# Optimization experiments

Measured on AMD Instinct MI355X. Metric: run time of the kernel, lower is better.

Reference implementation:

```python
import jax, jax.numpy as jnp
import numpy as np

DIM = 256
NEG_SLOPE = 0.01  # torch F.leaky_relu default


def setup_inputs() -> dict:
    key = jax.random.key(0)
    ks = jax.random.split(key, 10)
    B, O, I, D = 16, 64, 512, DIM
    q = jax.random.normal(ks[0], (B, O, D), dtype=jnp.float32)
    k = jax.random.normal(ks[1], (B, I, D), dtype=jnp.float32)
    v = jax.random.normal(ks[2], (B, I, D), dtype=jnp.float32)
    mask = jax.random.randint(ks[3], (B, I), 0, 2).astype(bool)  # 1/True = pad
    s = 1.0 / np.sqrt(2 * D)
    # score MLP: Linear(2D -> D), tanh, Linear(D -> 1)
    W1 = jax.random.normal(ks[4], (D, 2 * D), dtype=jnp.float32) * s
    b1 = jnp.zeros((D,), dtype=jnp.float32)
    W2 = jax.random.normal(ks[5], (1, D), dtype=jnp.float32) * (1.0 / np.sqrt(D))
    b2 = jnp.zeros((1,), dtype=jnp.float32)
    # output projection fw: Linear(D -> D)
    Wf = jax.random.normal(ks[6], (D, D), dtype=jnp.float32) * (1.0 / np.sqrt(D))
    bf = jnp.zeros((D,), dtype=jnp.float32)
    return {"q": q, "k": k, "v": v, "mask": mask,
            "W1": W1, "b1": b1, "W2": W2, "b2": b2, "Wf": Wf, "bf": bf}


def reference(q, k, v, mask, W1, b1, W2, b2, Wf, bf):
    # Linear over concat([q, k]) decomposes exactly: W1 @ [q;k] = W1q@q + W1k@k
    D = q.shape[-1]
    W1q, W1k = W1[:, :D], W1[:, D:]
    qp = jnp.einsum('bod,hd->boh', q, W1q)          # (B, O, D)
    kp = jnp.einsum('bid,hd->bih', k, W1k)          # (B, I, D)
    h = jnp.tanh(qp[:, :, None, :] + kp[:, None, :, :] + b1)  # (B, O, I, D)
    score = jnp.einsum('boih,h->boi', h, W2[0]) + b2[0]       # (B, O, I)
    score = jnp.where(mask[:, None, :], -jnp.inf, score)
    attn = jax.nn.softmax(score, axis=-1)           # (B, O, I)
    out = jnp.einsum('boi,bid->bod', attn, v)       # (B, O, D)
    out = out @ Wf.T + bf                           # dropout in eval mode = identity
    out = jnp.where(out >= 0, out, NEG_SLOPE * out) # leaky_relu
    return out, attn
```

## Files before the change

kernel.cpp:

```cpp
#include <hip/hip_runtime.h>
#include <math.h>

#define DIM 256
#define BATCH 16
#define NO 64
#define NI 512
#define NEG_SLOPE 0.01f
#define CSCALE 2.885390081777927f
#define OT 2

__global__ __launch_bounds__(256, 4) void proj_kernel(
    const float* __restrict__ q, const float* __restrict__ k,
    const float* __restrict__ W1, const float* __restrict__ b1,
    const float* __restrict__ Wf,
    float* __restrict__ Eq, float* __restrict__ Ek4, float* __restrict__ WfT)
{
  __shared__ float smem[8704];

  const int t  = threadIdx.x;
  const int bx = blockIdx.x;

  if (bx >= 576) {
    const int tt = bx - 576;
    const int tr = tt >> 2, tc = tt & 3;
#pragma unroll
    for (int p = 0; p < 4; ++p) {
      int idx = p * 256 + t;
      int row = idx >> 4, j = idx & 15;
      float4 vv = *(const float4*)(Wf + (size_t)(tr * 64 + row) * 256 + tc * 64 + j * 4);
      *(float4*)&smem[row * 68 + j * 4] = vv;
    }
    __syncthreads();
#pragma unroll
    for (int p = 0; p < 4; ++p) {
      int idx = p * 256 + t;
      int row = idx >> 4, j = idx & 15;
      float4 ov;
      ov.x = smem[(j * 4 + 0) * 68 + row];
      ov.y = smem[(j * 4 + 1) * 68 + row];
      ov.z = smem[(j * 4 + 2) * 68 + row];
      ov.w = smem[(j * 4 + 3) * 68 + row];
      *(float4*)(WfT + (size_t)(tc * 64 + row) * 256 + tr * 64 + j * 4) = ov;
    }
    return;
  }

  float* At = smem;
  float* Wt = smem + 4352;

  const int tx = t & 15;
  const int ty = t >> 4;
  const int mt = bx >> 2;
  const int nt = bx & 3;
  const int r0 = mt * 64;
  const int h0 = nt * 64;
  const bool isq = (r0 < BATCH * NO);
  const float* src = isq ? (q + (size_t)r0 * DIM)
                         : (k + (size_t)(r0 - BATCH * NO) * DIM);
  const int coff = isq ? 0 : DIM;

  float acc[4][4] = {};

  for (int c0 = 0; c0 < DIM; c0 += 64) {
    __syncthreads();
#pragma unroll
    for (int p = 0; p < 4; ++p) {
      int idx = p * 256 + t;
      int row = idx >> 4, j = idx & 15;
      float4 av = *(const float4*)(src + (size_t)row * DIM + c0 + j * 4);
      At[(4 * j + 0) * 68 + row] = av.x;
      At[(4 * j + 1) * 68 + row] = av.y;
      At[(4 * j + 2) * 68 + row] = av.z;
      At[(4 * j + 3) * 68 + row] = av.w;
      float4 wv = *(const float4*)(W1 + (size_t)(h0 + row) * (2 * DIM) + coff + c0 + j * 4);
      Wt[(4 * j + 0) * 68 + row] = wv.x;
      Wt[(4 * j + 1) * 68 + row] = wv.y;
      Wt[(4 * j + 2) * 68 + row] = wv.z;
      Wt[(4 * j + 3) * 68 + row] = wv.w;
    }
    __syncthreads();
#pragma unroll
    for (int dk = 0; dk < 64; ++dk) {
      float4 a4 = *(const float4*)&At[dk * 68 + ty * 4];
      float4 w4 = *(const float4*)&Wt[dk * 68 + tx * 4];
      const float ar[4] = {a4.x, a4.y, a4.z, a4.w};
      const float wr[4] = {w4.x, w4.y, w4.z, w4.w};
#pragma unroll
      for (int rr = 0; rr < 4; ++rr)
#pragma unroll
        for (int cc = 0; cc < 4; ++cc)
          acc[rr][cc] = fmaf(ar[rr], wr[cc], acc[rr][cc]);
    }
  }

  if (isq) {
    float4 bv = *(const float4*)(b1 + h0 + tx * 4);
    const float br[4] = {bv.x, bv.y, bv.z, bv.w};
#pragma unroll
    for (int rr = 0; rr < 4; ++rr) {
      int r = r0 + ty * 4 + rr;
      float4 ov;
      ov.x = __builtin_amdgcn_exp2f((acc[rr][0] + br[0]) * CSCALE);
      ov.y = __builtin_amdgcn_exp2f((acc[rr][1] + br[1]) * CSCALE);
      ov.z = __builtin_amdgcn_exp2f((acc[rr][2] + br[2]) * CSCALE);
      ov.w = __builtin_amdgcn_exp2f((acc[rr][3] + br[3]) * CSCALE);
      *(float4*)(Eq + (size_t)r * DIM + h0 + tx * 4) = ov;
    }
  } else {
    int ig0 = r0 - BATCH * NO;
    int b   = ig0 >> 9;
    int i0  = (ig0 & 511) + ty * 4;
    int hq0 = (h0 >> 2) + tx;
#pragma unroll
    for (int rr = 0; rr < 4; ++rr) {
      float4 ov;
      ov.x = __builtin_amdgcn_exp2f(acc[rr][0] * CSCALE);
      ov.y = __builtin_amdgcn_exp2f(acc[rr][1] * CSCALE);
      ov.z = __builtin_amdgcn_exp2f(acc[rr][2] * CSCALE);
      ov.w = __builtin_amdgcn_exp2f(acc[rr][3] * CSCALE);
      *(float4*)(Ek4 + ((size_t)(b * 64 + hq0) * NI + i0 + rr) * 4) = ov;
    }
  }
}

__device__ __forceinline__ void f4arr(float4 v, float* a) {
  a[0] = v.x; a[1] = v.y; a[2] = v.z; a[3] = v.w;
}

__global__ __launch_bounds__(512, 4) void attn_kernel(
    const float* __restrict__ Eq, const float* __restrict__ Ek4,
    const float* __restrict__ v, const int* __restrict__ mask,
    const float* __restrict__ W2, const float* __restrict__ b2,
    const float* __restrict__ WfT, const float* __restrict__ bf,
    float* __restrict__ out, float* __restrict__ attn_out)
{
  __shared__ float sc[OT][NI];
  __shared__ float pvp[8][OT][DIM];
  __shared__ float o0[OT][DIM];
  __shared__ float red4[8][OT];
  __shared__ float redw[8];

  const int t    = threadIdx.x;
  const int lane = t & 63;
  const int wid  = t >> 6;

  const int blk  = blockIdx.x;
  const int tile = (blk & 7) * 64 + (blk >> 3);
  const int b    = tile >> 5;
  const int bo0  = b * 64 + (tile & 31) * OT;

  float partial = (t < DIM) ? W2[t] : 0.f;
#pragma unroll
  for (int off = 32; off >= 1; off >>= 1) partial += __shfl_xor(partial, off, 64);
  if (lane == 0) redw[wid] = partial;
  __syncthreads();
  float sumw2 = 0.f;
#pragma unroll
  for (int w = 0; w < 8; ++w) sumw2 += redw[w];
  const float base = sumw2 + b2[0];

  const int i = t;
  const float4* kb4 = (const float4*)(Ek4 + (size_t)b * 64 * NI * 4);
  const float* qrow0 = Eq + (size_t)(bo0 + 0) * DIM;
  const float* qrow1 = Eq + (size_t)(bo0 + 1) * DIM;

  float acc0 = 0.f, acc1 = 0.f;
#pragma unroll 4
  for (int hq = 0; hq < 64; ++hq) {
    float4 kq = kb4[(size_t)hq * NI + i];
    float wr[4], q0r[4], q1r[4], kv[4];
    f4arr(*(const float4*)(W2 + hq * 4), wr);
    f4arr(*(const float4*)(qrow0 + hq * 4), q0r);
    f4arr(*(const float4*)(qrow1 + hq * 4), q1r);
    f4arr(kq, kv);
#pragma unroll
    for (int e = 0; e < 4; ++e) {
      float d0 = fmaf(q0r[e], kv[e], 1.f);
      acc0 = fmaf(wr[e], __builtin_amdgcn_rcpf(d0), acc0);
      float d1 = fmaf(q1r[e], kv[e], 1.f);
      acc1 = fmaf(wr[e], __builtin_amdgcn_rcpf(d1), acc1);
    }
  }

  const int mv = mask[(size_t)b * NI + i];
  float s0 = base - 2.f * acc0;
  float s1 = base - 2.f * acc1;
  if (mv) { s0 = -INFINITY; s1 = -INFINITY; }

  float m0 = s0, m1 = s1;
#pragma unroll
  for (int off = 32; off >= 1; off >>= 1) {
    m0 = fmaxf(m0, __shfl_xor(m0, off, 64));
    m1 = fmaxf(m1, __shfl_xor(m1, off, 64));
  }
  __syncthreads();
  if (lane == 0) { red4[wid][0] = m0; red4[wid][1] = m1; }
  __syncthreads();
  m0 = red4[0][0]; m1 = red4[0][1];
#pragma unroll
  for (int w = 1; w < 8; ++w) {
    m0 = fmaxf(m0, red4[w][0]);
    m1 = fmaxf(m1, red4[w][1]);
  }

  float p0 = __builtin_amdgcn_exp2f((s0 - m0) * 1.4426950408889634f);
  float p1 = __builtin_amdgcn_exp2f((s1 - m1) * 1.4426950408889634f);
  float ps0 = p0, ps1 = p1;
#pragma unroll
  for (int off = 32; off >= 1; off >>= 1) {
    ps0 += __shfl_xor(ps0, off, 64);
    ps1 += __shfl_xor(ps1, off, 64);
  }
  __syncthreads();
  if (lane == 0) { red4[wid][0] = ps0; red4[wid][1] = ps1; }
  __syncthreads();
  float ss0 = 0.f, ss1 = 0.f;
#pragma unroll
  for (int w = 0; w < 8; ++w) { ss0 += red4[w][0]; ss1 += red4[w][1]; }
  const float a0 = p0 * __builtin_amdgcn_rcpf(ss0);
  const float a1 = p1 * __builtin_amdgcn_rcpf(ss1);
  sc[0][i] = a0;
  sc[1][i] = a1;
  attn_out[(size_t)(bo0 + 0) * NI + i] = a0;
  attn_out[(size_t)(bo0 + 1) * NI + i] = a1;
  __syncthreads();

  {
    const int d4 = lane;
    float4 av0 = {0.f, 0.f, 0.f, 0.f};
    float4 av1 = {0.f, 0.f, 0.f, 0.f};
    const float4* vb4 = (const float4*)(v + (size_t)b * NI * DIM);
#pragma unroll 2
    for (int ib = wid * 64; ib < wid * 64 + 64; ib += 4) {
      float sa0[4], sa1[4];
      f4arr(*(const float4*)&sc[0][ib], sa0);
      f4arr(*(const float4*)&sc[1][ib], sa1);
#pragma unroll
      for (int j = 0; j < 4; ++j) {
        float4 vv = vb4[(size_t)(ib + j) * 64 + d4];
        av0.x = fmaf(sa0[j], vv.x, av0.x);
        av0.y = fmaf(sa0[j], vv.y, av0.y);
        av0.z = fmaf(sa0[j], vv.z, av0.z);
        av0.w = fmaf(sa0[j], vv.w, av0.w);
        av1.x = fmaf(sa1[j], vv.x, av1.x);
        av1.y = fmaf(sa1[j], vv.y, av1.y);
        av1.z = fmaf(sa1[j], vv.z, av1.z);
        av1.w = fmaf(sa1[j], vv.w, av1.w);
      }
    }
    *(float4*)&pvp[wid][0][d4 * 4] = av0;
    *(float4*)&pvp[wid][1][d4 * 4] = av1;
  }
  __syncthreads();
  {
    int oo = t >> 8, d = t & 255;
    float sacc = 0.f;
#pragma unroll
    for (int w = 0; w < 8; ++w) sacc += pvp[w][oo][d];
    o0[oo][d] = sacc;
  }
  __syncthreads();

  {
    const int oo = t >> 8;
    const int d  = t & 255;
    float f = 0.f;
#pragma unroll 8
    for (int e4 = 0; e4 < 64; ++e4) {
      float oa[4];
      f4arr(*(const float4*)&o0[oo][e4 * 4], oa);
#pragma unroll
      for (int c = 0; c < 4; ++c)
        f = fmaf(oa[c], WfT[(size_t)(e4 * 4 + c) * DIM + d], f);
    }
    f += bf[d];
    f = (f >= 0.f) ? f : NEG_SLOPE * f;
    out[(size_t)(bo0 + oo) * DIM + d] = f;
  }
}

extern "C" void kernel_launch(void* const* d_in, const int* in_sizes, int n_in,
                              void* d_out, int out_size, void* d_ws, size_t ws_size,
                              hipStream_t stream) {
  const float* q    = (const float*)d_in[0];
  const float* k    = (const float*)d_in[1];
  const float* v    = (const float*)d_in[2];
  const int*   mask = (const int*)d_in[3];
  const float* W1   = (const float*)d_in[4];
  const float* b1   = (const float*)d_in[5];
  const float* W2   = (const float*)d_in[6];
  const float* b2   = (const float*)d_in[7];
  const float* Wf   = (const float*)d_in[8];
  const float* bf   = (const float*)d_in[9];

  float* out      = (float*)d_out;
  float* attn_out = out + (size_t)BATCH * NO * DIM;

  float* Eq  = (float*)d_ws;
  float* Ek4 = Eq + (size_t)BATCH * NO * DIM;
  float* WfT = Ek4 + (size_t)BATCH * DIM * NI;

  proj_kernel<<<592, 256, 0, stream>>>(q, k, W1, b1, Wf, Eq, Ek4, WfT);
  attn_kernel<<<(BATCH * NO) / OT, 512, 0, stream>>>(Eq, Ek4, v, mask, W2, b2,
                                                     WfT, bf, out, attn_out);
}
```

Before: 143.9 us.

## Process four output rows per attention block and drop softmax max reduction

```diff
diff --git a/kernel.cpp b/kernel.cpp
--- a/kernel.cpp
+++ b/kernel.cpp
@@ -7,7 +7,7 @@
 #define NI 512
 #define NEG_SLOPE 0.01f
 #define CSCALE 2.885390081777927f
-#define OT 2
+#define OT 4
 
 __global__ __launch_bounds__(256, 4) void proj_kernel(
     const float* __restrict__ q, const float* __restrict__ k,
@@ -127,7 +127,7 @@
   a[0] = v.x; a[1] = v.y; a[2] = v.z; a[3] = v.w;
 }
 
-__global__ __launch_bounds__(512, 4) void attn_kernel(
+__global__ __launch_bounds__(512, 2) void attn_kernel(
     const float* __restrict__ Eq, const float* __restrict__ Ek4,
     const float* __restrict__ v, const int* __restrict__ mask,
     const float* __restrict__ W2, const float* __restrict__ b2,
@@ -145,9 +145,9 @@
   const int wid  = t >> 6;
 
   const int blk  = blockIdx.x;
-  const int tile = (blk & 7) * 64 + (blk >> 3);
-  const int b    = tile >> 5;
-  const int bo0  = b * 64 + (tile & 31) * OT;
+  const int tile = (blk & 7) * 32 + (blk >> 3);
+  const int b    = tile >> 4;
+  const int bo0  = b * 64 + (tile & 15) * OT;
 
   float partial = (t < DIM) ? W2[t] : 0.f;
 #pragma unroll
@@ -160,18 +160,22 @@
   const float base = sumw2 + b2[0];
 
   const int i = t;
-  const float4* kb4 = (const float4*)(Ek4 + (size_t)b * 64 * NI * 4);
+  const float4* kb4 = (const float4*)Ek4 + (size_t)b * 64 * NI;
   const float* qrow0 = Eq + (size_t)(bo0 + 0) * DIM;
   const float* qrow1 = Eq + (size_t)(bo0 + 1) * DIM;
-
-  float acc0 = 0.f, acc1 = 0.f;
+  const float* qrow2 = Eq + (size_t)(bo0 + 2) * DIM;
+  const float* qrow3 = Eq + (size_t)(bo0 + 3) * DIM;
+
+  float acc0 = 0.f, acc1 = 0.f, acc2 = 0.f, acc3 = 0.f;
 #pragma unroll 4
   for (int hq = 0; hq < 64; ++hq) {
     float4 kq = kb4[(size_t)hq * NI + i];
-    float wr[4], q0r[4], q1r[4], kv[4];
+    float wr[4], q0r[4], q1r[4], q2r[4], q3r[4], kv[4];
     f4arr(*(const float4*)(W2 + hq * 4), wr);
     f4arr(*(const float4*)(qrow0 + hq * 4), q0r);
     f4arr(*(const float4*)(qrow1 + hq * 4), q1r);
+    f4arr(*(const float4*)(qrow2 + hq * 4), q2r);
+    f4arr(*(const float4*)(qrow3 + hq * 4), q3r);
     f4arr(kq, kv);
 #pragma unroll
     for (int e = 0; e < 4; ++e) {
@@ -179,81 +183,77 @@
       acc0 = fmaf(wr[e], __builtin_amdgcn_rcpf(d0), acc0);
       float d1 = fmaf(q1r[e], kv[e], 1.f);
       acc1 = fmaf(wr[e], __builtin_amdgcn_rcpf(d1), acc1);
+      float d2 = fmaf(q2r[e], kv[e], 1.f);
+      acc2 = fmaf(wr[e], __builtin_amdgcn_rcpf(d2), acc2);
+      float d3 = fmaf(q3r[e], kv[e], 1.f);
+      acc3 = fmaf(wr[e], __builtin_amdgcn_rcpf(d3), acc3);
     }
   }
 
   const int mv = mask[(size_t)b * NI + i];
-  float s0 = base - 2.f * acc0;
-  float s1 = base - 2.f * acc1;
-  if (mv) { s0 = -INFINITY; s1 = -INFINITY; }
-
-  float m0 = s0, m1 = s1;
-#pragma unroll
-  for (int off = 32; off >= 1; off >>= 1) {
-    m0 = fmaxf(m0, __shfl_xor(m0, off, 64));
-    m1 = fmaxf(m1, __shfl_xor(m1, off, 64));
-  }
-  __syncthreads();
-  if (lane == 0) { red4[wid][0] = m0; red4[wid][1] = m1; }
-  __syncthreads();
-  m0 = red4[0][0]; m1 = red4[0][1];
-#pragma unroll
-  for (int w = 1; w < 8; ++w) {
-    m0 = fmaxf(m0, red4[w][0]);
-    m1 = fmaxf(m1, red4[w][1]);
-  }
-
-  float p0 = __builtin_amdgcn_exp2f((s0 - m0) * 1.4426950408889634f);
-  float p1 = __builtin_amdgcn_exp2f((s1 - m1) * 1.4426950408889634f);
-  float ps0 = p0, ps1 = p1;
-#pragma unroll
-  for (int off = 32; off >= 1; off >>= 1) {
-    ps0 += __shfl_xor(ps0, off, 64);
-    ps1 += __shfl_xor(ps1, off, 64);
-  }
-  __syncthreads();
-  if (lane == 0) { red4[wid][0] = ps0; red4[wid][1] = ps1; }
-  __syncthreads();
-  float ss0 = 0.f, ss1 = 0.f;
-#pragma unroll
-  for (int w = 0; w < 8; ++w) { ss0 += red4[w][0]; ss1 += red4[w][1]; }
-  const float a0 = p0 * __builtin_amdgcn_rcpf(ss0);
-  const float a1 = p1 * __builtin_amdgcn_rcpf(ss1);
-  sc[0][i] = a0;
-  sc[1][i] = a1;
-  attn_out[(size_t)(bo0 + 0) * NI + i] = a0;
-  attn_out[(size_t)(bo0 + 1) * NI + i] = a1;
+  float s[OT];
+  s[0] = base - 2.f * acc0;
+  s[1] = base - 2.f * acc1;
+  s[2] = base - 2.f * acc2;
+  s[3] = base - 2.f * acc3;
+  if (mv) { s[0] = -INFINITY; s[1] = -INFINITY; s[2] = -INFINITY; s[3] = -INFINITY; }
+
+  float p[OT], ps[OT];
+#pragma unroll
+  for (int oo = 0; oo < OT; ++oo) {
+    p[oo] = __builtin_amdgcn_exp2f(s[oo] * 1.4426950408889634f);
+    ps[oo] = p[oo];
+#pragma unroll
+    for (int off = 32; off >= 1; off >>= 1) ps[oo] += __shfl_xor(ps[oo], off, 64);
+  }
+  __syncthreads();
+  if (lane == 0) {
+#pragma unroll
+    for (int oo = 0; oo < OT; ++oo) red4[wid][oo] = ps[oo];
+  }
+  __syncthreads();
+#pragma unroll
+  for (int oo = 0; oo < OT; ++oo) {
+    float ss = 0.f;
+#pragma unroll
+    for (int w = 0; w < 8; ++w) ss += red4[w][oo];
+    float a = p[oo] * __builtin_amdgcn_rcpf(ss);
+    sc[oo][i] = a;
+    attn_out[(size_t)(bo0 + oo) * NI + i] = a;
+  }
   __syncthreads();
 
   {
     const int d4 = lane;
-    float4 av0 = {0.f, 0.f, 0.f, 0.f};
-    float4 av1 = {0.f, 0.f, 0.f, 0.f};
+    float4 av[OT];
+#pragma unroll
+    for (int oo = 0; oo < OT; ++oo) av[oo] = make_float4(0.f, 0.f, 0.f, 0.f);
     const float4* vb4 = (const float4*)(v + (size_t)b * NI * DIM);
 #pragma unroll 2
     for (int ib = wid * 64; ib < wid * 64 + 64; ib += 4) {
-      float sa0[4], sa1[4];
-      f4arr(*(const float4*)&sc[0][ib], sa0);
-      f4arr(*(const float4*)&sc[1][ib], sa1);
+      float sa[OT][4];
+#pragma unroll
+      for (int oo = 0; oo < OT; ++oo) f4arr(*(const float4*)&sc[oo][ib], sa[oo]);
 #pragma unroll
       for (int j = 0; j < 4; ++j) {
         float4 vv = vb4[(size_t)(ib + j) * 64 + d4];
-        av0.x = fmaf(sa0[j], vv.x, av0.x);
-        av0.y = fmaf(sa0[j], vv.y, av0.y);
-        av0.z = fmaf(sa0[j], vv.z, av0.z);
-        av0.w = fmaf(sa0[j], vv.w, av0.w);
-        av1.x = fmaf(sa1[j], vv.x, av1.x);
-        av1.y = fmaf(sa1[j], vv.y, av1.y);
-        av1.z = fmaf(sa1[j], vv.z, av1.z);
-        av1.w = fmaf(sa1[j], vv.w, av1.w);
+#pragma unroll
+        for (int oo = 0; oo < OT; ++oo) {
+          av[oo].x = fmaf(sa[oo][j], vv.x, av[oo].x);
+          av[oo].y = fmaf(sa[oo][j], vv.y, av[oo].y);
+          av[oo].z = fmaf(sa[oo][j], vv.z, av[oo].z);
+          av[oo].w = fmaf(sa[oo][j], vv.w, av[oo].w);
+        }
       }
     }
-    *(float4*)&pvp[wid][0][d4 * 4] = av0;
-    *(float4*)&pvp[wid][1][d4 * 4] = av1;
-  }
-  __syncthreads();
-  {
-    int oo = t >> 8, d = t & 255;
+#pragma unroll
+    for (int oo = 0; oo < OT; ++oo) *(float4*)&pvp[wid][oo][d4 * 4] = av[oo];
+  }
+  __syncthreads();
+#pragma unroll
+  for (int pp = 0; pp < 2; ++pp) {
+    int flat = pp * 512 + t;
+    int oo = flat >> 8, d = flat & 255;
     float sacc = 0.f;
 #pragma unroll
     for (int w = 0; w < 8; ++w) sacc += pvp[w][oo][d];
@@ -264,18 +264,25 @@
   {
     const int oo = t >> 8;
     const int d  = t & 255;
-    float f = 0.f;
-#pragma unroll 8
+    float f0 = 0.f, f1 = 0.f;
+#pragma unroll 4
     for (int e4 = 0; e4 < 64; ++e4) {
-      float oa[4];
+      float oa[4], ob[4];
       f4arr(*(const float4*)&o0[oo][e4 * 4], oa);
-#pragma unroll
-      for (int c = 0; c < 4; ++c)
-        f = fmaf(oa[c], WfT[(size_t)(e4 * 4 + c) * DIM + d], f);
-    }
-    f += bf[d];
-    f = (f >= 0.f) ? f : NEG_SLOPE * f;
-    out[(size_t)(bo0 + oo) * DIM + d] = f;
+      f4arr(*(const float4*)&o0[oo + 2][e4 * 4], ob);
+#pragma unroll
+      for (int c = 0; c < 4; ++c) {
+        float wv = WfT[(size_t)(e4 * 4 + c) * DIM + d];
+        f0 = fmaf(oa[c], wv, f0);
+        f1 = fmaf(ob[c], wv, f1);
+      }
+    }
+    float bfv = bf[d];
+    f0 += bfv; f1 += bfv;
+    f0 = (f0 >= 0.f) ? f0 : NEG_SLOPE * f0;
+    f1 = (f1 >= 0.f) ? f1 : NEG_SLOPE * f1;
+    out[(size_t)(bo0 + oo) * DIM + d]     = f0;
+    out[(size_t)(bo0 + oo + 2) * DIM + d] = f1;
   }
 }
 
```

Result: no change. 145.6 us (+1.2%).
